# Kernel optimization log

Measured on AMD Instinct MI355X. Metric: run time of the kernel, lower is better.

Reference implementation:

```python
import jax, jax.numpy as jnp
import numpy as np

N_NODES = 100000
N_EDGES = 1000000
D_FEAT = 64


def setup_inputs() -> dict:
    key = jax.random.key(0)
    k1, k2, k3, k4 = jax.random.split(key, 4)
    feat = jax.random.normal(k1, (N_NODES, D_FEAT), dtype=jnp.float32)
    edge_weight = jax.random.uniform(k2, (N_EDGES,), dtype=jnp.float32)
    edge_src = jax.random.randint(k3, (N_EDGES,), 0, N_NODES, dtype=jnp.int64)
    edge_dst = jax.random.randint(k4, (N_EDGES,), 0, N_NODES, dtype=jnp.int64)
    return {"feat": feat, "edge_weight": edge_weight,
            "edge_src": edge_src, "edge_dst": edge_dst}


def reference(feat, edge_weight, edge_src, edge_dst):
    # Original module reverses edges: graph((edges()[1], edges()[0])), then
    # u_mul_e('h','_edge_weight') + sum. So in terms of the ORIGINAL edge
    # orientation (edge_src -> edge_dst):
    #   out[edge_src] += feat[edge_dst] * edge_weight
    msgs = feat[edge_dst] * edge_weight[:, None]          # [E, D] gather + scale
    out = jax.ops.segment_sum(msgs, edge_src, num_segments=feat.shape[0])
    return out
```

## Files before the change

### kernel.cpp

```cpp
#include <hip/hip_runtime.h>


#define D_FEAT    64
#define SB        512
#define SB_SHIFT  9
#define CAPB      6144
#define BIN_CHUNK 4096
#define BIN_THR   512
#define CONV_BLK  128

typedef int      v2i __attribute__((ext_vector_type(2)));
typedef unsigned v4u __attribute__((ext_vector_type(4)));
typedef float    v4f __attribute__((ext_vector_type(4)));

__device__ __forceinline__ ushort f2bf(float f) {
    unsigned u = __float_as_uint(f);
    unsigned r = (u + 0x7fff + ((u >> 16) & 1)) >> 16;
    return (ushort)r;
}
__device__ __forceinline__ float bf_lo(unsigned u) { return __uint_as_float(u << 16); }
__device__ __forceinline__ float bf_hi(unsigned u) { return __uint_as_float(u & 0xffff0000u); }

__global__ __launch_bounds__(BIN_THR) void bin_conv(
    const float* __restrict__ feat, ushort* __restrict__ fh, int total4,
    const int* __restrict__ src, const int* __restrict__ dst,
    const float* __restrict__ w, int* __restrict__ cursor,
    long long* __restrict__ ep, int E, int NB, int nbin)
{
    if ((int)blockIdx.x >= nbin) {
        int cb = blockIdx.x - nbin;
        for (int i = cb * BIN_THR + threadIdx.x; i < total4; i += CONV_BLK * BIN_THR) {
            float4 v = reinterpret_cast<const float4*>(feat)[i];
            ushort4 o;
            o.x = f2bf(v.x); o.y = f2bf(v.y); o.z = f2bf(v.z); o.w = f2bf(v.w);
            reinterpret_cast<ushort4*>(fh)[i] = o;
        }
        return;
    }
    extern __shared__ int sh[];
    int* cnt   = sh;
    int* basel = sh + NB;
    int* stage = sh + 2 * NB;
    for (int b = threadIdx.x; b < NB; b += BIN_THR) cnt[b] = 0;
    __syncthreads();
    int start = blockIdx.x * BIN_CHUNK;
    int end   = min(start + BIN_CHUNK, E);
    for (int e = start + threadIdx.x; e < end; e += BIN_THR) {
        int s = src[e];
        stage[e - start] = s;
        atomicAdd(&cnt[s >> SB_SHIFT], 1);
    }
    __syncthreads();
    for (int b = threadIdx.x; b < NB; b += BIN_THR) {
        int c = cnt[b];
        basel[b] = c ? atomicAdd(&cursor[b], c) : 0;
    }
    __syncthreads();
    for (int b = threadIdx.x; b < NB; b += BIN_THR) cnt[b] = 0;
    __syncthreads();
    for (int e = start + threadIdx.x; e < end; e += BIN_THR) {
        int s  = stage[e - start];
        int b  = s >> SB_SHIFT;
        int ls = s & (SB - 1);
        int r  = atomicAdd(&cnt[b], 1);
        unsigned px = (unsigned)(dst[e] | (ls << 17));
        unsigned wb = __float_as_uint(w[e]);
        ep[(size_t)b * CAPB + basel[b] + r] =
            (long long)(((unsigned long long)wb << 32) | px);
    }
}

__global__ __launch_bounds__(512) void node_sort(
    const int* __restrict__ cursor, long long* __restrict__ ep,
    v2i* __restrict__ node_rng, int N)
{
    __shared__ long long eb[CAPB];
    __shared__ int cnt[SB];
    __shared__ int cur[SB];
    __shared__ int wpre[8];
    int b = blockIdx.x, t = threadIdx.x;
    cnt[t] = 0;
    __syncthreads();
    int sz = min(cursor[b], CAPB);
    int base = b * CAPB;
    for (int i = t; i < sz; i += 512) {
        long long e = ep[base + i];
        eb[i] = e;
        atomicAdd(&cnt[((int)(unsigned)e >> 17) & (SB - 1)], 1);
    }
    __syncthreads();
    int c = cnt[t];
    int lane = t & 63, wv = t >> 6;
    int x = c;
    #pragma unroll
    for (int d = 1; d < 64; d <<= 1) {
        int y = __shfl_up(x, d, 64);
        if (lane >= d) x += y;
    }
    if (lane == 63) wpre[wv] = x;
    __syncthreads();
    if (t == 0) {
        int run = 0;
        #pragma unroll
        for (int k = 0; k < 8; k++) { int v = wpre[k]; wpre[k] = run; run += v; }
    }
    __syncthreads();
    int excl = x - c + wpre[wv];
    cur[t] = excl;
    int node = b * SB + t;
    if (node < N) {
        v2i rng; rng.x = base + excl; rng.y = base + excl + c;
        node_rng[node] = rng;
    }
    __syncthreads();
    for (int i = t; i < sz; i += 512) {
        long long e = eb[i];
        unsigned px = (unsigned)e;
        int ls  = (int)(px >> 17) & (SB - 1);
        int pos = atomicAdd(&cur[ls], 1);
        ep[base + pos] = (long long)((e & 0xffffffff00000000ull) | (px & 0x1FFFFu));
    }
}

__global__ __launch_bounds__(256) void segment_bf16(
    const ushort* __restrict__ fh, const v2i* __restrict__ node_rng,
    const long long* __restrict__ ep, float* __restrict__ out, int N)
{
    int tid  = blockIdx.x * blockDim.x + threadIdx.x;
    int node = tid >> 3;
    int q    = tid & 7;
    if (node >= N) return;
    v2i rng = node_rng[node];
    int j = rng.x, end = rng.y;
    float a0 = 0.f, a1 = 0.f, a2 = 0.f, a3 = 0.f;
    float a4 = 0.f, a5 = 0.f, a6 = 0.f, a7 = 0.f;
    for (; j + 4 <= end; j += 4) {
        long long e0 = ep[j],     e1 = ep[j + 1];
        long long e2 = ep[j + 2], e3 = ep[j + 3];
        v4u h0 = *reinterpret_cast<const v4u*>(&fh[(size_t)(unsigned)(e0 & 0x1FFFF) * D_FEAT + q * 8]);
        v4u h1 = *reinterpret_cast<const v4u*>(&fh[(size_t)(unsigned)(e1 & 0x1FFFF) * D_FEAT + q * 8]);
        v4u h2 = *reinterpret_cast<const v4u*>(&fh[(size_t)(unsigned)(e2 & 0x1FFFF) * D_FEAT + q * 8]);
        v4u h3 = *reinterpret_cast<const v4u*>(&fh[(size_t)(unsigned)(e3 & 0x1FFFF) * D_FEAT + q * 8]);
        float w0 = __uint_as_float((unsigned)((unsigned long long)e0 >> 32));
        float w1 = __uint_as_float((unsigned)((unsigned long long)e1 >> 32));
        float w2 = __uint_as_float((unsigned)((unsigned long long)e2 >> 32));
        float w3 = __uint_as_float((unsigned)((unsigned long long)e3 >> 32));
        a0 += bf_lo(h0.x) * w0; a1 += bf_hi(h0.x) * w0;
        a2 += bf_lo(h0.y) * w0; a3 += bf_hi(h0.y) * w0;
        a4 += bf_lo(h0.z) * w0; a5 += bf_hi(h0.z) * w0;
        a6 += bf_lo(h0.w) * w0; a7 += bf_hi(h0.w) * w0;
        a0 += bf_lo(h1.x) * w1; a1 += bf_hi(h1.x) * w1;
        a2 += bf_lo(h1.y) * w1; a3 += bf_hi(h1.y) * w1;
        a4 += bf_lo(h1.z) * w1; a5 += bf_hi(h1.z) * w1;
        a6 += bf_lo(h1.w) * w1; a7 += bf_hi(h1.w) * w1;
        a0 += bf_lo(h2.x) * w2; a1 += bf_hi(h2.x) * w2;
        a2 += bf_lo(h2.y) * w2; a3 += bf_hi(h2.y) * w2;
        a4 += bf_lo(h2.z) * w2; a5 += bf_hi(h2.z) * w2;
        a6 += bf_lo(h2.w) * w2; a7 += bf_hi(h2.w) * w2;
        a0 += bf_lo(h3.x) * w3; a1 += bf_hi(h3.x) * w3;
        a2 += bf_lo(h3.y) * w3; a3 += bf_hi(h3.y) * w3;
        a4 += bf_lo(h3.z) * w3; a5 += bf_hi(h3.z) * w3;
        a6 += bf_lo(h3.w) * w3; a7 += bf_hi(h3.w) * w3;
    }
    for (; j < end; j++) {
        long long e = ep[j];
        v4u h = *reinterpret_cast<const v4u*>(&fh[(size_t)(unsigned)(e & 0x1FFFF) * D_FEAT + q * 8]);
        float ww = __uint_as_float((unsigned)((unsigned long long)e >> 32));
        a0 += bf_lo(h.x) * ww; a1 += bf_hi(h.x) * ww;
        a2 += bf_lo(h.y) * ww; a3 += bf_hi(h.y) * ww;
        a4 += bf_lo(h.z) * ww; a5 += bf_hi(h.z) * ww;
        a6 += bf_lo(h.w) * ww; a7 += bf_hi(h.w) * ww;
    }
    float* o = &out[(size_t)node * D_FEAT + q * 8];
    *reinterpret_cast<v4f*>(o)     = v4f{a0, a1, a2, a3};
    *reinterpret_cast<v4f*>(o + 4) = v4f{a4, a5, a6, a7};
}

extern "C" void kernel_launch(void* const* d_in, const int* in_sizes, int n_in,
                              void* d_out, int out_size, void* d_ws, size_t ws_size,
                              hipStream_t stream) {
    const float* feat = (const float*)d_in[0];
    const float* w    = (const float*)d_in[1];
    const int*   src  = (const int*)d_in[2];
    const int*   dst  = (const int*)d_in[3];
    float* out = (float*)d_out;

    int N  = out_size / D_FEAT;
    int E  = in_sizes[1];
    int NB = (N + SB - 1) / SB;

    int* cursor   = (int*)d_ws;
    v2i* node_rng = (v2i*)(cursor + ((NB + 1) & ~1));
    uintptr_t ap = ((uintptr_t)(node_rng + N) + 15) & ~(uintptr_t)15;
    long long* ep = (long long*)ap;
    ushort* fh = (ushort*)(ep + (size_t)NB * CAPB);

    (void)hipMemsetAsync(cursor, 0, (size_t)NB * sizeof(int), stream);

    int nbin = (E + BIN_CHUNK - 1) / BIN_CHUNK;
    size_t lds_bin = (2 * (size_t)NB + BIN_CHUNK) * sizeof(int);
    int total4 = N * D_FEAT / 4;

    bin_conv<<<nbin + CONV_BLK, BIN_THR, lds_bin, stream>>>(
        feat, fh, total4, src, dst, w, cursor, ep, E, NB, nbin);
    node_sort<<<NB, 512, 0, stream>>>(cursor, ep, node_rng, N);

    long long segthreads = (long long)N * 8;
    segment_bf16<<<(int)((segthreads + 255) / 256), 256, 0, stream>>>(
        fh, node_rng, ep, out, N);
}
```

Baseline: 72.24 us.

## Reuse atomic ranks in binning/sort and split segment sum into feature halves

The binning kernel now keeps the rank returned by the first shared-memory atomic, packed into the staged source index, so the second counter reset and second atomic pass are gone. node_sort likewise stores each edge's rank in a ushort LDS array and computes the output position as prefix plus rank, with no atomics in the scatter. The segment kernel is split into two launches, each covering 32 of the 64 features with 4 threads per node. The split is meant to shrink the gather working set per pass for better L2 locality, at the cost of reading the edge list twice and an extra launch.

```diff
diff --git a/kernel.cpp b/kernel.cpp
--- a/kernel.cpp
+++ b/kernel.cpp
@@ -47,8 +47,8 @@
     int end   = min(start + BIN_CHUNK, E);
     for (int e = start + threadIdx.x; e < end; e += BIN_THR) {
         int s = src[e];
-        stage[e - start] = s;
-        atomicAdd(&cnt[s >> SB_SHIFT], 1);
+        int r = atomicAdd(&cnt[s >> SB_SHIFT], 1);
+        stage[e - start] = s | (r << 17);
     }
     __syncthreads();
     for (int b = threadIdx.x; b < NB; b += BIN_THR) {
@@ -56,13 +56,12 @@
         basel[b] = c ? atomicAdd(&cursor[b], c) : 0;
     }
     __syncthreads();
-    for (int b = threadIdx.x; b < NB; b += BIN_THR) cnt[b] = 0;
-    __syncthreads();
     for (int e = start + threadIdx.x; e < end; e += BIN_THR) {
-        int s  = stage[e - start];
+        int sr = stage[e - start];
+        int s  = sr & 0x1FFFF;
+        int r  = (int)((unsigned)sr >> 17);
         int b  = s >> SB_SHIFT;
         int ls = s & (SB - 1);
-        int r  = atomicAdd(&cnt[b], 1);
         unsigned px = (unsigned)(dst[e] | (ls << 17));
         unsigned wb = __float_as_uint(w[e]);
         ep[(size_t)b * CAPB + basel[b] + r] =
@@ -75,9 +74,9 @@
     v2i* __restrict__ node_rng, int N)
 {
     __shared__ long long eb[CAPB];
-    __shared__ int cnt[SB];
-    __shared__ int cur[SB];
-    __shared__ int wpre[8];
+    __shared__ ushort   rnk[CAPB];
+    __shared__ int      cnt[SB];
+    __shared__ int      wpre[8];
     int b = blockIdx.x, t = threadIdx.x;
     cnt[t] = 0;
     __syncthreads();
@@ -86,7 +85,8 @@
     for (int i = t; i < sz; i += 512) {
         long long e = ep[base + i];
         eb[i] = e;
-        atomicAdd(&cnt[((int)(unsigned)e >> 17) & (SB - 1)], 1);
+        int r = atomicAdd(&cnt[((int)(unsigned)e >> 17) & (SB - 1)], 1);
+        rnk[i] = (ushort)r;
     }
     __syncthreads();
     int c = cnt[t];
@@ -106,30 +106,31 @@
     }
     __syncthreads();
     int excl = x - c + wpre[wv];
-    cur[t] = excl;
     int node = b * SB + t;
     if (node < N) {
         v2i rng; rng.x = base + excl; rng.y = base + excl + c;
         node_rng[node] = rng;
     }
+    cnt[t] = excl;
     __syncthreads();
     for (int i = t; i < sz; i += 512) {
         long long e = eb[i];
         unsigned px = (unsigned)e;
         int ls  = (int)(px >> 17) & (SB - 1);
-        int pos = atomicAdd(&cur[ls], 1);
+        int pos = cnt[ls] + rnk[i];
         ep[base + pos] = (long long)((e & 0xffffffff00000000ull) | (px & 0x1FFFFu));
     }
 }
 
-__global__ __launch_bounds__(256) void segment_bf16(
+__global__ __launch_bounds__(256) void segment_half(
     const ushort* __restrict__ fh, const v2i* __restrict__ node_rng,
-    const long long* __restrict__ ep, float* __restrict__ out, int N)
+    const long long* __restrict__ ep, float* __restrict__ out, int N, int half)
 {
     int tid  = blockIdx.x * blockDim.x + threadIdx.x;
-    int node = tid >> 3;
-    int q    = tid & 7;
+    int node = tid >> 2;
+    int q    = tid & 3;
     if (node >= N) return;
+    int foff = half * 32 + q * 8;
     v2i rng = node_rng[node];
     int j = rng.x, end = rng.y;
     float a0 = 0.f, a1 = 0.f, a2 = 0.f, a3 = 0.f;
@@ -137,10 +138,10 @@
     for (; j + 4 <= end; j += 4) {
         long long e0 = ep[j],     e1 = ep[j + 1];
         long long e2 = ep[j + 2], e3 = ep[j + 3];
-        v4u h0 = *reinterpret_cast<const v4u*>(&fh[(size_t)(unsigned)(e0 & 0x1FFFF) * D_FEAT + q * 8]);
-        v4u h1 = *reinterpret_cast<const v4u*>(&fh[(size_t)(unsigned)(e1 & 0x1FFFF) * D_FEAT + q * 8]);
-        v4u h2 = *reinterpret_cast<const v4u*>(&fh[(size_t)(unsigned)(e2 & 0x1FFFF) * D_FEAT + q * 8]);
-        v4u h3 = *reinterpret_cast<const v4u*>(&fh[(size_t)(unsigned)(e3 & 0x1FFFF) * D_FEAT + q * 8]);
+        v4u h0 = *reinterpret_cast<const v4u*>(&fh[(size_t)(unsigned)(e0 & 0x1FFFF) * D_FEAT + foff]);
+        v4u h1 = *reinterpret_cast<const v4u*>(&fh[(size_t)(unsigned)(e1 & 0x1FFFF) * D_FEAT + foff]);
+        v4u h2 = *reinterpret_cast<const v4u*>(&fh[(size_t)(unsigned)(e2 & 0x1FFFF) * D_FEAT + foff]);
+        v4u h3 = *reinterpret_cast<const v4u*>(&fh[(size_t)(unsigned)(e3 & 0x1FFFF) * D_FEAT + foff]);
         float w0 = __uint_as_float((unsigned)((unsigned long long)e0 >> 32));
         float w1 = __uint_as_float((unsigned)((unsigned long long)e1 >> 32));
         float w2 = __uint_as_float((unsigned)((unsigned long long)e2 >> 32));
@@ -164,14 +165,14 @@
     }
     for (; j < end; j++) {
         long long e = ep[j];
-        v4u h = *reinterpret_cast<const v4u*>(&fh[(size_t)(unsigned)(e & 0x1FFFF) * D_FEAT + q * 8]);
+        v4u h = *reinterpret_cast<const v4u*>(&fh[(size_t)(unsigned)(e & 0x1FFFF) * D_FEAT + foff]);
         float ww = __uint_as_float((unsigned)((unsigned long long)e >> 32));
         a0 += bf_lo(h.x) * ww; a1 += bf_hi(h.x) * ww;
         a2 += bf_lo(h.y) * ww; a3 += bf_hi(h.y) * ww;
         a4 += bf_lo(h.z) * ww; a5 += bf_hi(h.z) * ww;
         a6 += bf_lo(h.w) * ww; a7 += bf_hi(h.w) * ww;
     }
-    float* o = &out[(size_t)node * D_FEAT + q * 8];
+    float* o = &out[(size_t)node * D_FEAT + foff];
     *reinterpret_cast<v4f*>(o)     = v4f{a0, a1, a2, a3};
     *reinterpret_cast<v4f*>(o + 4) = v4f{a4, a5, a6, a7};
 }
@@ -205,7 +206,8 @@
         feat, fh, total4, src, dst, w, cursor, ep, E, NB, nbin);
     node_sort<<<NB, 512, 0, stream>>>(cursor, ep, node_rng, N);
 
-    long long segthreads = (long long)N * 8;
-    segment_bf16<<<(int)((segthreads + 255) / 256), 256, 0, stream>>>(
-        fh, node_rng, ep, out, N);
-}
+    long long segthreads = (long long)N * 4;
+    int segblk = (int)((segthreads + 255) / 256);
+    segment_half<<<segblk, 256, 0, stream>>>(fh, node_rng, ep, out, N, 0);
+    segment_half<<<segblk, 256, 0, stream>>>(fh, node_rng, ep, out, N, 1);
+}
```

After: 92.26 us. 1.28x slower.
